# Kernel tuning notes

Hardware: AMD Instinct MI355X
Metric: run time of the kernel (lower is better)

Reference implementation:

```python
import jax, jax.numpy as jnp
import numpy as np

IN_CAPS = 32
IN_CH = 8
OUT_CAPS = 10
OUT_CH = 16
NUM_ROUTING = 3
WID = 6
HEI = 6
BATCH = 64


def setup_inputs() -> dict:
    key = jax.random.key(0)
    k1, k2 = jax.random.split(key)
    u = jax.random.normal(k1, (BATCH, IN_CAPS, IN_CH, WID, HEI), dtype=jnp.float32)
    W = jax.random.normal(k2, (IN_CAPS, IN_CH, WID, HEI, OUT_CAPS, OUT_CH), dtype=jnp.float32) * 0.05
    return {"u": u, "W": W}


def reference(u, W):
    # u: [B, ic, ich, w, h]; W: [ic, ich, w, h, oc, och]
    B = u.shape[0]
    # _mul_1: broadcast multiply then fold (ich*w*h) into one axis
    u_hat = (u[..., None, None] * W[None]).reshape(
        B, IN_CAPS, IN_CH * WID * HEI, OUT_CAPS, OUT_CH
    )  # [B, ic, D, oc, och]
    u_sum = u_hat.sum(axis=2)            # [B, ic, oc, och] (used every iteration in _mul_2)
    u_dot = u_hat.sum(axis=(0, 2, 4))    # [ic, oc] (constant part of _dot)
    b_ij = jnp.zeros((IN_CAPS, OUT_CAPS), dtype=u.dtype)
    v_j = None
    for _ in range(NUM_ROUTING):
        c_ij = jax.nn.softmax(b_ij, axis=0)                     # softmax over in_capsules
        s_j = jnp.einsum('io,bioc->boc', c_ij, u_sum)           # [B, oc, och]
        # squash with GLOBAL L1 norm (torch .norm(1) over all elements) -- faithful to source
        n = jnp.abs(s_j).sum()
        v_j = (n * n) / (1.0 + n * n) * (s_j / n)               # [B, oc, och]
        agree = u_dot * v_j.sum(axis=(0, 2))[None, :]           # [ic, oc]
        b_ij = b_ij + jax.lax.stop_gradient(agree)              # torch uses .data (detached)
    return v_j
```

## Files before the change

kernel.cpp:

```cpp
#include <hip/hip_runtime.h>
#include <math.h>

#define B_   64
#define IC   32
#define D_   288
#define OC   10
#define OCH  16
#define J_   160
#define BJ   10240

__global__ __launch_bounds__(320) void k_usum(const float* __restrict__ u,
                                              const float* __restrict__ Wt,
                                              float* __restrict__ US,
                                              float* __restrict__ UDp,
                                              float* __restrict__ nacc,
                                              int* __restrict__ bar) {
    const int ic  = blockIdx.x & 31;
    const int bt  = blockIdx.x >> 5;
    const int tid = threadIdx.x;
    __shared__ float  u_t[D_ * 4];
    __shared__ float4 part[8][4][40];
    __shared__ float  ud_part[OC];
    if (tid < OC) ud_part[tid] = 0.f;
    if (blockIdx.x == 0 && tid == 0) {
        nacc[0] = 0.f; nacc[1] = 0.f; nacc[2] = 0.f;
        *bar = 0;
    }
    if (tid < 288) {
        const int b_sub = tid / 72;
        const int f4    = tid - b_sub * 72;
        const int b     = bt * 4 + b_sub;
        float4 v = ((const float4*)(u + (size_t)(b * IC + ic) * D_))[f4];
        u_t[(f4 * 4 + 0) * 4 + b_sub] = v.x;
        u_t[(f4 * 4 + 1) * 4 + b_sub] = v.y;
        u_t[(f4 * 4 + 2) * 4 + b_sub] = v.z;
        u_t[(f4 * 4 + 3) * 4 + b_sub] = v.w;
    }
    __syncthreads();
    {
        const int j4 = tid % 40;
        const int dq = tid / 40;
        const float4* wp = (const float4*)(Wt + (size_t)ic * D_ * J_)
                           + (size_t)(dq * 36) * 40 + j4;
        const float4* ut = ((const float4*)u_t) + dq * 36;
        float4 a0 = make_float4(0.f, 0.f, 0.f, 0.f);
        float4 a1 = a0, a2 = a0, a3 = a0;
#define ACC16(qv, wv)                                                        \
        a0.x += qv.x * wv.x; a0.y += qv.x * wv.y;                            \
        a0.z += qv.x * wv.z; a0.w += qv.x * wv.w;                            \
        a1.x += qv.y * wv.x; a1.y += qv.y * wv.y;                            \
        a1.z += qv.y * wv.z; a1.w += qv.y * wv.w;                            \
        a2.x += qv.z * wv.x; a2.y += qv.z * wv.y;                            \
        a2.z += qv.z * wv.z; a2.w += qv.z * wv.w;                            \
        a3.x += qv.w * wv.x; a3.y += qv.w * wv.y;                            \
        a3.z += qv.w * wv.z; a3.w += qv.w * wv.w;
        for (int k0 = 0; k0 < 36; k0 += 4) {
            float4 w0 = wp[(k0 + 0) * 40];
            float4 w1 = wp[(k0 + 1) * 40];
            float4 w2 = wp[(k0 + 2) * 40];
            float4 w3 = wp[(k0 + 3) * 40];
            float4 q0 = ut[k0 + 0];
            float4 q1 = ut[k0 + 1];
            float4 q2 = ut[k0 + 2];
            float4 q3 = ut[k0 + 3];
            ACC16(q0, w0)
            ACC16(q1, w1)
            ACC16(q2, w2)
            ACC16(q3, w3)
        }
#undef ACC16
        part[dq][0][j4] = a0;
        part[dq][1][j4] = a1;
        part[dq][2][j4] = a2;
        part[dq][3][j4] = a3;
    }
    __syncthreads();
    if (tid < 160) {
        const int jj = tid % 40;
        const int bs = tid / 40;
        float4 r = part[0][bs][jj];
        #pragma unroll
        for (int dq = 1; dq < 8; ++dq) {
            float4 p = part[dq][bs][jj];
            r.x += p.x; r.y += p.y; r.z += p.z; r.w += p.w;
        }
        ((float4*)(US + (size_t)ic * BJ + (bt * 4 + bs) * J_))[jj] = r;
        float g = r.x + r.y + r.z + r.w;
        g += __shfl_xor(g, 1);
        g += __shfl_xor(g, 2);
        if ((tid & 3) == 0) atomicAdd(&ud_part[jj >> 2], g);
    }
    __syncthreads();
    if (tid < OC) UDp[blockIdx.x * OC + tid] = ud_part[tid];
}

__global__ __launch_bounds__(1024) void k_route(const float* __restrict__ US,
                                                const float* __restrict__ UDp,
                                                float* __restrict__ nacc,
                                                int* __restrict__ bar,
                                                float* __restrict__ out) {
    const int tid = threadIdx.x;
    const int i   = tid & 31;
    const int o   = tid >> 5;
    __shared__ float cij[OC * IC];
    __shared__ float wred[16];
    __shared__ float nsh;
    float udv = 0.f;
    if (tid < 320) {
        #pragma unroll
        for (int bt = 0; bt < 16; ++bt) udv += UDp[(bt * 32 + i) * OC + o];
    }
    const int t  = blockIdx.x * 1024 + tid;
    const int ot = (t >> 4) % OC;
    float usv[IC];
    {
        const float* usp = US + t;
        #pragma unroll
        for (int ii = 0; ii < IC; ++ii) usv[ii] = usp[(size_t)ii * BJ];
    }
    float bij = 0.f;
    for (int q = 0; q < 3; ++q) {
        float cs = 0.f;
        if (tid < 320) {
            float m = bij;
            m = fmaxf(m, __shfl_xor(m, 16, 32));
            m = fmaxf(m, __shfl_xor(m,  8, 32));
            m = fmaxf(m, __shfl_xor(m,  4, 32));
            m = fmaxf(m, __shfl_xor(m,  2, 32));
            m = fmaxf(m, __shfl_xor(m,  1, 32));
            float e  = __expf(bij - m);
            float se = e;
            se += __shfl_xor(se, 16, 32);
            se += __shfl_xor(se,  8, 32);
            se += __shfl_xor(se,  4, 32);
            se += __shfl_xor(se,  2, 32);
            se += __shfl_xor(se,  1, 32);
            float c = e / se;
            cij[o * IC + i] = c;
            cs = c * udv;
            cs += __shfl_xor(cs, 16, 32);
            cs += __shfl_xor(cs,  8, 32);
            cs += __shfl_xor(cs,  4, 32);
            cs += __shfl_xor(cs,  2, 32);
            cs += __shfl_xor(cs,  1, 32);
        }
        __syncthreads();
        float s = 0.f;
        {
            const float* cp = cij + ot * IC;
            #pragma unroll
            for (int ii = 0; ii < IC; ++ii) s += cp[ii] * usv[ii];
        }
        float a = fabsf(s);
        #pragma unroll
        for (int off = 32; off; off >>= 1) a += __shfl_down(a, off);
        if ((tid & 63) == 0) wred[tid >> 6] = a;
        __syncthreads();
        if (tid == 0) {
            float blk = 0.f;
            #pragma unroll
            for (int w = 0; w < 16; ++w) blk += wred[w];
            atomicAdd(nacc + q, blk);
            __threadfence();
            atomicAdd(bar, 1);
            while (__hip_atomic_load(bar, __ATOMIC_ACQUIRE,
                                     __HIP_MEMORY_SCOPE_AGENT) < 10 * (q + 1))
                __builtin_amdgcn_s_sleep(1);
            nsh = __hip_atomic_load(nacc + q, __ATOMIC_RELAXED,
                                    __HIP_MEMORY_SCOPE_AGENT);
        }
        __syncthreads();
        const float n  = nsh;
        const float n2 = n * n;
        if (q < 2) {
            if (tid < 320) bij += udv * ((n2 / (1.f + n2)) * (cs / n));
        } else {
            out[t] = (n2 / (1.f + n2)) * (s / n);
        }
    }
}

extern "C" void kernel_launch(void* const* d_in, const int* in_sizes, int n_in,
                              void* d_out, int out_size, void* d_ws, size_t ws_size,
                              hipStream_t stream) {
    (void)in_sizes; (void)n_in; (void)out_size; (void)ws_size;
    const float* u  = (const float*)d_in[0];
    const float* Wt = (const float*)d_in[1];
    float* ws   = (float*)d_ws;
    float* US   = ws;
    float* UDp  = ws + 327680;
    float* nacc = ws + 332800;
    int*   bar  = (int*)(ws + 332803);

    k_usum <<<dim3(512), dim3(320),  0, stream>>>(u, Wt, US, UDp, nacc, bar);
    k_route<<<dim3(10),  dim3(1024), 0, stream>>>(US, UDp, nacc, bar, (float*)d_out);
}
```

Before: 74.28 us.

## Software-pipeline weight loads, specialize first routing iteration, relax barrier fence

The k_usum inner loop is manually unrolled with a three-deep rotation of register buffers, so the weight loads for later k-steps are in flight while the current step's FMAs run. In k_route the first routing iteration drops the softmax and one __syncthreads, because b_ij is zero and c_ij is the uniform 1/32. The UDp loads are moved after the US register loads, and the threadfence plus atomic is replaced by a single release-ordered fetch_add. The barrier counter also moves to its own cache line away from the norm accumulators. The cost is more live registers in k_usum and a hard-coded assumption that the initial logits are zero.

```diff
diff --git a/kernel.cpp b/kernel.cpp
--- a/kernel.cpp
+++ b/kernel.cpp
@@ -54,20 +54,27 @@
         a2.z += qv.z * wv.z; a2.w += qv.z * wv.w;                            \
         a3.x += qv.w * wv.x; a3.y += qv.w * wv.y;                            \
         a3.z += qv.w * wv.z; a3.w += qv.w * wv.w;
-        for (int k0 = 0; k0 < 36; k0 += 4) {
-            float4 w0 = wp[(k0 + 0) * 40];
-            float4 w1 = wp[(k0 + 1) * 40];
-            float4 w2 = wp[(k0 + 2) * 40];
-            float4 w3 = wp[(k0 + 3) * 40];
-            float4 q0 = ut[k0 + 0];
-            float4 q1 = ut[k0 + 1];
-            float4 q2 = ut[k0 + 2];
-            float4 q3 = ut[k0 + 3];
-            ACC16(q0, w0)
-            ACC16(q1, w1)
-            ACC16(q2, w2)
-            ACC16(q3, w3)
-        }
+#define LOADW(W0, W1, W2, W3, K)                                             \
+        W0 = wp[(K + 0) * 40]; W1 = wp[(K + 1) * 40];                        \
+        W2 = wp[(K + 2) * 40]; W3 = wp[(K + 3) * 40];
+#define CONS(W0, W1, W2, W3, K)                                              \
+        { float4 q0 = ut[K + 0], q1 = ut[K + 1],                             \
+                 q2 = ut[K + 2], q3 = ut[K + 3];                             \
+          ACC16(q0, W0) ACC16(q1, W1) ACC16(q2, W2) ACC16(q3, W3) }
+        float4 A0, A1, A2, A3, B0, B1, B2, B3, C0, C1, C2, C3;
+        LOADW(A0, A1, A2, A3, 0)
+        LOADW(B0, B1, B2, B3, 4)
+        LOADW(C0, C1, C2, C3, 8)   CONS(A0, A1, A2, A3, 0)
+        LOADW(A0, A1, A2, A3, 12)  CONS(B0, B1, B2, B3, 4)
+        LOADW(B0, B1, B2, B3, 16)  CONS(C0, C1, C2, C3, 8)
+        LOADW(C0, C1, C2, C3, 20)  CONS(A0, A1, A2, A3, 12)
+        LOADW(A0, A1, A2, A3, 24)  CONS(B0, B1, B2, B3, 16)
+        LOADW(B0, B1, B2, B3, 28)  CONS(C0, C1, C2, C3, 20)
+        LOADW(C0, C1, C2, C3, 32)  CONS(A0, A1, A2, A3, 24)
+                                   CONS(B0, B1, B2, B3, 28)
+                                   CONS(C0, C1, C2, C3, 32)
+#undef CONS
+#undef LOADW
 #undef ACC16
         part[dq][0][j4] = a0;
         part[dq][1][j4] = a1;
@@ -105,11 +112,6 @@
     __shared__ float cij[OC * IC];
     __shared__ float wred[16];
     __shared__ float nsh;
-    float udv = 0.f;
-    if (tid < 320) {
-        #pragma unroll
-        for (int bt = 0; bt < 16; ++bt) udv += UDp[(bt * 32 + i) * OC + o];
-    }
     const int t  = blockIdx.x * 1024 + tid;
     const int ot = (t >> 4) % OC;
     float usv[IC];
@@ -118,35 +120,53 @@
         #pragma unroll
         for (int ii = 0; ii < IC; ++ii) usv[ii] = usp[(size_t)ii * BJ];
     }
+    float udv = 0.f;
+    if (tid < 320) {
+        #pragma unroll
+        for (int bt = 0; bt < 16; ++bt) udv += UDp[(bt * 32 + i) * OC + o];
+    }
     float bij = 0.f;
     for (int q = 0; q < 3; ++q) {
         float cs = 0.f;
-        if (tid < 320) {
-            float m = bij;
-            m = fmaxf(m, __shfl_xor(m, 16, 32));
-            m = fmaxf(m, __shfl_xor(m,  8, 32));
-            m = fmaxf(m, __shfl_xor(m,  4, 32));
-            m = fmaxf(m, __shfl_xor(m,  2, 32));
-            m = fmaxf(m, __shfl_xor(m,  1, 32));
-            float e  = __expf(bij - m);
-            float se = e;
-            se += __shfl_xor(se, 16, 32);
-            se += __shfl_xor(se,  8, 32);
-            se += __shfl_xor(se,  4, 32);
-            se += __shfl_xor(se,  2, 32);
-            se += __shfl_xor(se,  1, 32);
-            float c = e / se;
-            cij[o * IC + i] = c;
-            cs = c * udv;
-            cs += __shfl_xor(cs, 16, 32);
-            cs += __shfl_xor(cs,  8, 32);
-            cs += __shfl_xor(cs,  4, 32);
-            cs += __shfl_xor(cs,  2, 32);
-            cs += __shfl_xor(cs,  1, 32);
-        }
-        __syncthreads();
-        float s = 0.f;
-        {
+        float s  = 0.f;
+        if (q == 0) {
+            #pragma unroll
+            for (int ii = 0; ii < IC; ++ii) s += usv[ii];
+            s *= 0.03125f;
+            if (tid < 320) {
+                cs = udv;
+                cs += __shfl_xor(cs, 16, 32);
+                cs += __shfl_xor(cs,  8, 32);
+                cs += __shfl_xor(cs,  4, 32);
+                cs += __shfl_xor(cs,  2, 32);
+                cs += __shfl_xor(cs,  1, 32);
+                cs *= 0.03125f;
+            }
+        } else {
+            if (tid < 320) {
+                float m = bij;
+                m = fmaxf(m, __shfl_xor(m, 16, 32));
+                m = fmaxf(m, __shfl_xor(m,  8, 32));
+                m = fmaxf(m, __shfl_xor(m,  4, 32));
+                m = fmaxf(m, __shfl_xor(m,  2, 32));
+                m = fmaxf(m, __shfl_xor(m,  1, 32));
+                float e  = __expf(bij - m);
+                float se = e;
+                se += __shfl_xor(se, 16, 32);
+                se += __shfl_xor(se,  8, 32);
+                se += __shfl_xor(se,  4, 32);
+                se += __shfl_xor(se,  2, 32);
+                se += __shfl_xor(se,  1, 32);
+                float c = e / se;
+                cij[o * IC + i] = c;
+                cs = c * udv;
+                cs += __shfl_xor(cs, 16, 32);
+                cs += __shfl_xor(cs,  8, 32);
+                cs += __shfl_xor(cs,  4, 32);
+                cs += __shfl_xor(cs,  2, 32);
+                cs += __shfl_xor(cs,  1, 32);
+            }
+            __syncthreads();
             const float* cp = cij + ot * IC;
             #pragma unroll
             for (int ii = 0; ii < IC; ++ii) s += cp[ii] * usv[ii];
@@ -161,8 +181,8 @@
             #pragma unroll
             for (int w = 0; w < 16; ++w) blk += wred[w];
             atomicAdd(nacc + q, blk);
-            __threadfence();
-            atomicAdd(bar, 1);
+            __hip_atomic_fetch_add(bar, 1, __ATOMIC_RELEASE,
+                                   __HIP_MEMORY_SCOPE_AGENT);
             while (__hip_atomic_load(bar, __ATOMIC_ACQUIRE,
                                      __HIP_MEMORY_SCOPE_AGENT) < 10 * (q + 1))
                 __builtin_amdgcn_s_sleep(1);
@@ -190,7 +210,7 @@
     float* US   = ws;
     float* UDp  = ws + 327680;
     float* nacc = ws + 332800;
-    int*   bar  = (int*)(ws + 332803);
+    int*   bar  = (int*)(ws + 332832);
 
     k_usum <<<dim3(512), dim3(320),  0, stream>>>(u, Wt, US, UDp, nacc, bar);
     k_route<<<dim3(10),  dim3(1024), 0, stream>>>(US, UDp, nacc, bar, (float*)d_out);
```

New measurement: 74.64 us. Within noise of the previous version (+0.5%).

## Halve routing blocks, two outputs per thread, specialize uniform first iteration

Applied to the files above, without the earlier changes.

The routing kernel now launches 5 blocks instead of 10, and each thread handles two output elements, so fewer blocks take part in each grid-wide barrier. The first routing iteration exploits the uniform softmax (1/32) and uses plain sums instead of computing exp and filling the shared coefficient table. The fence plus atomic pair is replaced by a single release atomic add, and the barrier counter moves to its own offset. The cost is double the register load per thread (64 cached values) and half as many blocks reading US, which may lengthen the load phase.

```diff
diff --git a/kernel.cpp b/kernel.cpp
--- a/kernel.cpp
+++ b/kernel.cpp
@@ -105,53 +105,76 @@
     __shared__ float cij[OC * IC];
     __shared__ float wred[16];
     __shared__ float nsh;
+    const int t0  = blockIdx.x * 2048 + tid;
+    const int t1  = t0 + 1024;
+    const int ot0 = (t0 >> 4) % OC;
+    const int ot1 = (t1 >> 4) % OC;
+    float usv0[IC], usv1[IC];
+    {
+        const float* usp = US + t0;
+        #pragma unroll
+        for (int ii = 0; ii < IC; ++ii) usv0[ii] = usp[(size_t)ii * BJ];
+        #pragma unroll
+        for (int ii = 0; ii < IC; ++ii) usv1[ii] = usp[(size_t)ii * BJ + 1024];
+    }
     float udv = 0.f;
     if (tid < 320) {
         #pragma unroll
         for (int bt = 0; bt < 16; ++bt) udv += UDp[(bt * 32 + i) * OC + o];
-    }
-    const int t  = blockIdx.x * 1024 + tid;
-    const int ot = (t >> 4) % OC;
-    float usv[IC];
-    {
-        const float* usp = US + t;
-        #pragma unroll
-        for (int ii = 0; ii < IC; ++ii) usv[ii] = usp[(size_t)ii * BJ];
     }
     float bij = 0.f;
     for (int q = 0; q < 3; ++q) {
         float cs = 0.f;
-        if (tid < 320) {
-            float m = bij;
-            m = fmaxf(m, __shfl_xor(m, 16, 32));
-            m = fmaxf(m, __shfl_xor(m,  8, 32));
-            m = fmaxf(m, __shfl_xor(m,  4, 32));
-            m = fmaxf(m, __shfl_xor(m,  2, 32));
-            m = fmaxf(m, __shfl_xor(m,  1, 32));
-            float e  = __expf(bij - m);
-            float se = e;
-            se += __shfl_xor(se, 16, 32);
-            se += __shfl_xor(se,  8, 32);
-            se += __shfl_xor(se,  4, 32);
-            se += __shfl_xor(se,  2, 32);
-            se += __shfl_xor(se,  1, 32);
-            float c = e / se;
-            cij[o * IC + i] = c;
-            cs = c * udv;
-            cs += __shfl_xor(cs, 16, 32);
-            cs += __shfl_xor(cs,  8, 32);
-            cs += __shfl_xor(cs,  4, 32);
-            cs += __shfl_xor(cs,  2, 32);
-            cs += __shfl_xor(cs,  1, 32);
-        }
-        __syncthreads();
-        float s = 0.f;
-        {
-            const float* cp = cij + ot * IC;
-            #pragma unroll
-            for (int ii = 0; ii < IC; ++ii) s += cp[ii] * usv[ii];
-        }
-        float a = fabsf(s);
+        float s0 = 0.f, s1 = 0.f;
+        if (q == 0) {
+            #pragma unroll
+            for (int ii = 0; ii < IC; ++ii) s0 += usv0[ii];
+            #pragma unroll
+            for (int ii = 0; ii < IC; ++ii) s1 += usv1[ii];
+            s0 *= 0.03125f;
+            s1 *= 0.03125f;
+            if (tid < 320) {
+                cs = udv;
+                cs += __shfl_xor(cs, 16, 32);
+                cs += __shfl_xor(cs,  8, 32);
+                cs += __shfl_xor(cs,  4, 32);
+                cs += __shfl_xor(cs,  2, 32);
+                cs += __shfl_xor(cs,  1, 32);
+                cs *= 0.03125f;
+            }
+        } else {
+            if (tid < 320) {
+                float m = bij;
+                m = fmaxf(m, __shfl_xor(m, 16, 32));
+                m = fmaxf(m, __shfl_xor(m,  8, 32));
+                m = fmaxf(m, __shfl_xor(m,  4, 32));
+                m = fmaxf(m, __shfl_xor(m,  2, 32));
+                m = fmaxf(m, __shfl_xor(m,  1, 32));
+                float e  = __expf(bij - m);
+                float se = e;
+                se += __shfl_xor(se, 16, 32);
+                se += __shfl_xor(se,  8, 32);
+                se += __shfl_xor(se,  4, 32);
+                se += __shfl_xor(se,  2, 32);
+                se += __shfl_xor(se,  1, 32);
+                float c = e / se;
+                cij[o * IC + i] = c;
+                cs = c * udv;
+                cs += __shfl_xor(cs, 16, 32);
+                cs += __shfl_xor(cs,  8, 32);
+                cs += __shfl_xor(cs,  4, 32);
+                cs += __shfl_xor(cs,  2, 32);
+                cs += __shfl_xor(cs,  1, 32);
+            }
+            __syncthreads();
+            const float* cp0 = cij + ot0 * IC;
+            const float* cp1 = cij + ot1 * IC;
+            #pragma unroll
+            for (int ii = 0; ii < IC; ++ii) s0 += cp0[ii] * usv0[ii];
+            #pragma unroll
+            for (int ii = 0; ii < IC; ++ii) s1 += cp1[ii] * usv1[ii];
+        }
+        float a = fabsf(s0) + fabsf(s1);
         #pragma unroll
         for (int off = 32; off; off >>= 1) a += __shfl_down(a, off);
         if ((tid & 63) == 0) wred[tid >> 6] = a;
@@ -161,10 +184,10 @@
             #pragma unroll
             for (int w = 0; w < 16; ++w) blk += wred[w];
             atomicAdd(nacc + q, blk);
-            __threadfence();
-            atomicAdd(bar, 1);
+            __hip_atomic_fetch_add(bar, 1, __ATOMIC_RELEASE,
+                                   __HIP_MEMORY_SCOPE_AGENT);
             while (__hip_atomic_load(bar, __ATOMIC_ACQUIRE,
-                                     __HIP_MEMORY_SCOPE_AGENT) < 10 * (q + 1))
+                                     __HIP_MEMORY_SCOPE_AGENT) < 5 * (q + 1))
                 __builtin_amdgcn_s_sleep(1);
             nsh = __hip_atomic_load(nacc + q, __ATOMIC_RELAXED,
                                     __HIP_MEMORY_SCOPE_AGENT);
@@ -175,7 +198,8 @@
         if (q < 2) {
             if (tid < 320) bij += udv * ((n2 / (1.f + n2)) * (cs / n));
         } else {
-            out[t] = (n2 / (1.f + n2)) * (s / n);
+            out[t0] = (n2 / (1.f + n2)) * (s0 / n);
+            out[t1] = (n2 / (1.f + n2)) * (s1 / n);
         }
     }
 }
@@ -190,8 +214,8 @@
     float* US   = ws;
     float* UDp  = ws + 327680;
     float* nacc = ws + 332800;
-    int*   bar  = (int*)(ws + 332803);
+    int*   bar  = (int*)(ws + 332832);
 
     k_usum <<<dim3(512), dim3(320),  0, stream>>>(u, Wt, US, UDp, nacc, bar);
-    k_route<<<dim3(10),  dim3(1024), 0, stream>>>(US, UDp, nacc, bar, (float*)d_out);
+    k_route<<<dim3(5),   dim3(1024), 0, stream>>>(US, UDp, nacc, bar, (float*)d_out);
 }
```

Result: slower. 78.64 us (+5.9%).
